# Kernel tuning notes

Measured on AMD Instinct MI355X. Metric: run time of the kernel, lower is better.

The kernel has to match this reference:

```python
import jax, jax.numpy as jnp
import numpy as np

MIN_NORM = 1e-15
PROJ_EPS = 4e-3  # float32 boundary eps used by hgcn PoincareBall.proj
C = 1.0          # curvature for every layer
N, E, D = 10000, 320000, 256


def _norm(x):
    return jnp.maximum(jnp.linalg.norm(x, axis=-1, keepdims=True), MIN_NORM)


def artanh(x):
    return jnp.arctanh(jnp.clip(x, -1 + 1e-7, 1 - 1e-7))


def proj(x, c):
    norm = _norm(x)
    maxnorm = (1.0 - PROJ_EPS) / jnp.sqrt(c)
    return jnp.where(norm > maxnorm, x / norm * maxnorm, x)


def expmap0(u, c):
    sqrt_c = jnp.sqrt(c)
    u_norm = _norm(u)
    return jnp.tanh(sqrt_c * u_norm) * u / (sqrt_c * u_norm)


def logmap0(p, c):
    sqrt_c = jnp.sqrt(c)
    p_norm = _norm(p)
    return artanh(sqrt_c * p_norm) * p / (sqrt_c * p_norm)


def mobius_add(x, y, c):
    x2 = jnp.sum(x * x, -1, keepdims=True)
    y2 = jnp.sum(y * y, -1, keepdims=True)
    xy = jnp.sum(x * y, -1, keepdims=True)
    num = (1 + 2 * c * xy + c * y2) * x + (1 - c * x2) * y
    denom = 1 + 2 * c * xy + c * c * x2 * y2
    return num / jnp.maximum(denom, MIN_NORM)


def mobius_matvec(m, x, c):
    sqrt_c = jnp.sqrt(c)
    x_norm = _norm(x)
    mx = x @ m.T
    mx_norm = _norm(mx)
    res = jnp.tanh(mx_norm / x_norm * artanh(sqrt_c * x_norm)) * mx / (mx_norm * sqrt_c)
    zero_row = jnp.all(mx == 0, axis=-1, keepdims=True)
    return jnp.where(zero_row, jnp.zeros_like(res), res)


def hgc_layer(h, W, b, edge_weight, edge_src, edge_dst, c):
    # HypLinear (dropout=0, eval mode)
    res = proj(mobius_matvec(W, h, c), c)
    hyp_bias = proj(expmap0(b[None, :], c), c)
    h = proj(mobius_add(res, hyp_bias, c), c)
    # HypAgg: tangent-space neighborhood aggregation (spmm over edge list)
    xt = logmap0(h, c)                                  # [N, D]
    msgs = edge_weight[:, None] * xt[edge_src]          # [E, D] irregular gather
    agg = jax.ops.segment_sum(msgs, edge_dst, num_segments=N)
    h = proj(expmap0(agg, c), c)
    # HypAct: relu in tangent space, map back with c_out
    xt = jax.nn.relu(logmap0(h, c))
    return proj(expmap0(xt, c), c)


def setup_inputs() -> dict:
    key = jax.random.key(0)
    ks = jax.random.split(key, 8)
    x = jax.random.normal(ks[0], (N, D), dtype=jnp.float32)
    edge_src = jax.random.randint(ks[1], (E,), 0, N)
    edge_dst = jax.random.randint(ks[2], (E,), 0, N)
    # normalized-adjacency-like positive weights (~1/deg scale)
    edge_weight = jax.random.uniform(ks[3], (E,), dtype=jnp.float32) / 32.0
    s = 1.0 / np.sqrt(D)
    W1 = jax.random.normal(ks[4], (D, D), dtype=jnp.float32) * s
    b1 = jnp.zeros((D,), dtype=jnp.float32)
    W2 = jax.random.normal(ks[5], (D, D), dtype=jnp.float32) * s
    b2 = jnp.zeros((D,), dtype=jnp.float32)
    return {"x": x, "W1": W1, "b1": b1, "W2": W2, "b2": b2,
            "edge_weight": edge_weight, "edge_src": edge_src, "edge_dst": edge_dst}


def reference(x, W1, b1, W2, b2, edge_weight, edge_src, edge_dst):
    # old=True path: map Euclidean features onto the Poincare ball first
    h = proj(expmap0(x, C), C)
    h = hgc_layer(h, W1, b1, edge_weight, edge_src, edge_dst, C)
    h = hgc_layer(h, W2, b2, edge_weight, edge_src, edge_dst, C)
    return h
```

## Files before the change

### kernel.cpp

```cpp
#include <hip/hip_runtime.h>
#include <hip/hip_fp16.h>

#define DIM 256
#define MAXNORM 0.996f
#define MINN 1e-15f
#define CLIPV 0.9999999f
#define CAP 128
#define LDW 264

typedef __attribute__((ext_vector_type(8))) short bf16x8;
typedef __attribute__((ext_vector_type(4))) float f32x4;

__device__ __forceinline__ unsigned short f2bf(float f) {
    unsigned int u = __float_as_uint(f);
    u += 0x7fffu + ((u >> 16) & 1u);
    return (unsigned short)(u >> 16);
}
__device__ __forceinline__ float h2f(unsigned short h) {
    return __half2float(__ushort_as_half(h));
}
__device__ __forceinline__ unsigned short f2h(float f) {
    return __half_as_ushort(__float2half(f));
}
__device__ __forceinline__ float wsum(float v) {
    v += __shfl_xor(v, 32);
    v += __shfl_xor(v, 16);
    v += __shfl_xor(v, 8);
    v += __shfl_xor(v, 4);
    v += __shfl_xor(v, 2);
    v += __shfl_xor(v, 1);
    return v;
}
__device__ __forceinline__ float gsum16(float v) {
    v += __shfl_xor(v, 8);
    v += __shfl_xor(v, 4);
    v += __shfl_xor(v, 2);
    v += __shfl_xor(v, 1);
    return v;
}

__global__ void k_setup(const float* __restrict__ x, unsigned short* __restrict__ h_bf,
                        float* __restrict__ hnorm2, int nrows,
                        int* __restrict__ cnt,
                        const float* __restrict__ W1, const float* __restrict__ W2,
                        unsigned short* __restrict__ w_bf, int nPerW, int eB) {
    int bid = blockIdx.x;
    if (bid < eB) {
        int gid = bid * 256 + threadIdx.x;
        int row = gid >> 6, lane = gid & 63;
        if (row >= nrows) return;
        size_t base = (size_t)row * DIM + lane * 4;
        float4 v = *(const float4*)(x + base);
        float ss = wsum(v.x * v.x + v.y * v.y + v.z * v.z + v.w * v.w);
        float n = fmaxf(sqrtf(ss), MINN);
        float tn = tanhf(n);
        float hn = (tn > MAXNORM) ? MAXNORM : tn;
        float s = hn / n;
        ushort4 ob;
        ob.x = f2bf(v.x * s); ob.y = f2bf(v.y * s);
        ob.z = f2bf(v.z * s); ob.w = f2bf(v.w * s);
        *(ushort4*)(h_bf + base) = ob;
        if (lane == 0) hnorm2[row] = hn * hn;
    } else if (bid < eB + 8) {
        int i = (bid - eB) * 256 + threadIdx.x;
        int stride = 8 * 256;
        for (; i < nrows; i += stride) cnt[i] = 0;
    } else {
        int i = (bid - eB - 8) * 256 + threadIdx.x;
        int stride = 128 * 256;
        for (; i < 2 * nPerW; i += stride)
            w_bf[i] = f2bf(i < nPerW ? W1[i] : W2[i - nPerW]);
    }
}

__global__ void k_fill(const int* __restrict__ esrc, const int* __restrict__ edst,
                       const float* __restrict__ ew, int* __restrict__ cnt,
                       int2* __restrict__ bucket, int nE, int nrows) {
    int e = blockIdx.x * blockDim.x + threadIdx.x;
    if (e >= nE) return;
    int d = edst[e];
    if (d < 0 || d >= nrows) return;
    int pos = atomicAdd(&cnt[d], 1);
    if (pos < CAP)
        bucket[(size_t)d * CAP + pos] = make_int2(esrc[e], __float_as_int(ew[e]));
}

__global__ void k_gemm_post(const unsigned short* __restrict__ Abf,
                            const unsigned short* __restrict__ Wbf,
                            const float* __restrict__ hnorm2,
                            const float* __restrict__ bias,
                            unsigned short* __restrict__ XT, int M) {
    int wave = threadIdx.x >> 6;
    int lane = threadIdx.x & 63;
    int r = lane & 15, oct = lane >> 4;
    int i0 = (blockIdx.x * 4 + wave) * 16;
    int arow = i0 + r;
    bool av = arow < M;
    const unsigned short* ap = Abf + (size_t)(av ? arow : 0) * DIM + oct * 8;
    const unsigned short* wp = Wbf + (size_t)r * DIM + oct * 8;
    const bf16x8 zf = {0, 0, 0, 0, 0, 0, 0, 0};
    f32x4 acc[16];
#pragma unroll
    for (int jt = 0; jt < 16; ++jt) acc[jt] = (f32x4){0.f, 0.f, 0.f, 0.f};
    for (int k0 = 0; k0 < 256; k0 += 32) {
        bf16x8 a = av ? *(const bf16x8*)(ap + k0) : zf;
#pragma unroll
        for (int jt = 0; jt < 16; ++jt) {
            bf16x8 w = *(const bf16x8*)(wp + (size_t)jt * 16 * DIM + k0);
            acc[jt] = __builtin_amdgcn_mfma_f32_16x16x32_bf16(a, w, acc[jt], 0, 0, 0);
        }
    }
    float bv[16];
    float bss = 0.f;
#pragma unroll
    for (int jt = 0; jt < 16; ++jt) {
        bv[jt] = bias[jt * 16 + r];
        bss = fmaf(bv[jt], bv[jt], bss);
    }
    bss = gsum16(bss);
    float bn = fmaxf(sqrtf(bss), MINN);
    float btn = tanhf(bn);
    float bhn = (btn > MAXNORM) ? MAXNORM : btn;
    float bscale = bhn / bn;
    float y2 = bhn * bhn;
#pragma unroll
    for (int jt = 0; jt < 16; ++jt) bv[jt] *= bscale;

#pragma unroll
    for (int q = 0; q < 4; ++q) {
        int row = i0 + oct * 4 + q;
        float sm = 0.f, sxy = 0.f;
#pragma unroll
        for (int jt = 0; jt < 16; ++jt) {
            float m = acc[jt][q];
            sm  = fmaf(m, m, sm);
            sxy = fmaf(m, bv[jt], sxy);
        }
        sm = gsum16(sm);
        sxy = gsum16(sxy);
        if (row < M) {
            float sh = hnorm2[row];
            float xn = fmaxf(sqrtf(sh), MINN);
            float at = atanhf(fminf(xn, CLIPV));
            float mn = fmaxf(sqrtf(sm), MINN);
            float t = tanhf(mn / xn * at);
            float alpha = t / mn;
            float resn = t;
            if (t > MAXNORM) { alpha = MAXNORM / mn; resn = MAXNORM; }
            float x2 = resn * resn;
            float xy = alpha * sxy;
            float Aa = 1.f + 2.f * xy + y2;
            float Bb = 1.f - x2;
            float den = fmaxf(1.f + 2.f * xy + x2 * y2, MINN);
            float s_m = Aa * alpha / den;
            float s_b = Bb / den;
            float hn2 = (Aa * Aa * x2 + 2.f * Aa * Bb * xy + Bb * Bb * y2) / (den * den);
            float hn = fmaxf(sqrtf(fmaxf(hn2, 0.f)), MINN);
            if (hn > MAXNORM) { float f = MAXNORM / hn; s_m *= f; s_b *= f; hn = MAXNORM; }
            float lt = atanhf(fminf(hn, CLIPV)) / hn;
            s_m *= lt; s_b *= lt;
#pragma unroll
            for (int jt = 0; jt < 16; ++jt)
                XT[(size_t)row * DIM + jt * 16 + r] = f2h(fmaf(s_m, acc[jt][q], s_b * bv[jt]));
        }
    }
}

__global__ void __launch_bounds__(256) k_fused(
                        const unsigned short* __restrict__ XT,
                        const int* __restrict__ cnt, const int2* __restrict__ bucket,
                        const unsigned short* __restrict__ Wbf,
                        const float* __restrict__ bias,
                        unsigned short* __restrict__ XT2, int M) {
    __shared__ unsigned short ldsA[16][LDW];
    __shared__ float lds_hn2[16];
    __shared__ float lds_sm[4][16];
    __shared__ float lds_sxy[4][16];
    int wave = threadIdx.x >> 6;
    int lane = threadIdx.x & 63;
    int i0 = blockIdx.x * 16;

    for (int i = 0; i < 4; ++i) {
        int row16 = wave * 4 + i;
        int row = i0 + row16;
        if (row >= M) continue;
        int deg = cnt[row];
        if (deg > CAP) deg = CAP;
        const int2* cpk = bucket + (size_t)row * CAP;
        float a0 = 0.f, a1 = 0.f, a2 = 0.f, a3 = 0.f;
        int p = 0;
        for (; p + 7 < deg; p += 8) {
            ushort4 v[8];
            float w[8];
#pragma unroll
            for (int u = 0; u < 8; ++u) {
                int2 pk = cpk[p + u];
                w[u] = __int_as_float(pk.y);
                v[u] = *(const ushort4*)(XT + (size_t)pk.x * DIM + lane * 4);
            }
#pragma unroll
            for (int u = 0; u < 8; ++u) {
                a0 = fmaf(w[u], h2f(v[u].x), a0);
                a1 = fmaf(w[u], h2f(v[u].y), a1);
                a2 = fmaf(w[u], h2f(v[u].z), a2);
                a3 = fmaf(w[u], h2f(v[u].w), a3);
            }
        }
        for (; p < deg; ++p) {
            int2 pk = cpk[p];
            float w = __int_as_float(pk.y);
            ushort4 v = *(const ushort4*)(XT + (size_t)pk.x * DIM + lane * 4);
            a0 = fmaf(w, h2f(v.x), a0); a1 = fmaf(w, h2f(v.y), a1);
            a2 = fmaf(w, h2f(v.z), a2); a3 = fmaf(w, h2f(v.w), a3);
        }
        float ss = wsum(a0 * a0 + a1 * a1 + a2 * a2 + a3 * a3);
        float n = fmaxf(sqrtf(ss), MINN);
        float tn = tanhf(n);
        float hn = (tn > MAXNORM) ? MAXNORM : tn;
        float s1 = hn / n;
        float lt = atanhf(fminf(hn, CLIPV)) / fmaxf(hn, MINN);
        float s2 = lt * s1;
        float x0 = fmaxf(s2 * a0, 0.f), x1 = fmaxf(s2 * a1, 0.f);
        float x2 = fmaxf(s2 * a2, 0.f), x3 = fmaxf(s2 * a3, 0.f);
        float ss2 = wsum(x0 * x0 + x1 * x1 + x2 * x2 + x3 * x3);
        float n2 = fmaxf(sqrtf(ss2), MINN);
        float tn2 = tanhf(n2);
        float hn2c = (tn2 > MAXNORM) ? MAXNORM : tn2;
        float s3 = hn2c / n2;
        ushort4 ob;
        ob.x = f2bf(s3 * x0); ob.y = f2bf(s3 * x1);
        ob.z = f2bf(s3 * x2); ob.w = f2bf(s3 * x3);
        *(ushort4*)&ldsA[row16][lane * 4] = ob;
        if (lane == 0) lds_hn2[row16] = hn2c * hn2c;
    }
    __syncthreads();

    int r = lane & 15, oct = lane >> 4;
    int jtbase = wave * 4;
    const unsigned short* wp = Wbf + (size_t)(jtbase * 16 + r) * DIM + oct * 8;
    f32x4 acc[4];
#pragma unroll
    for (int j = 0; j < 4; ++j) acc[j] = (f32x4){0.f, 0.f, 0.f, 0.f};
#pragma unroll
    for (int k0 = 0; k0 < 256; k0 += 32) {
        bf16x8 a = *(const bf16x8*)&ldsA[r][oct * 8 + k0];
#pragma unroll
        for (int j = 0; j < 4; ++j) {
            bf16x8 w = *(const bf16x8*)(wp + (size_t)j * 16 * DIM + k0);
            acc[j] = __builtin_amdgcn_mfma_f32_16x16x32_bf16(a, w, acc[j], 0, 0, 0);
        }
    }
    float bss = 0.f;
#pragma unroll
    for (int jt = 0; jt < 16; ++jt) {
        float b = bias[jt * 16 + r];
        bss = fmaf(b, b, bss);
    }
    bss = gsum16(bss);
    float bn = fmaxf(sqrtf(bss), MINN);
    float btn = tanhf(bn);
    float bhn = (btn > MAXNORM) ? MAXNORM : btn;
    float bscale = bhn / bn;
    float y2 = bhn * bhn;
    float bvw[4];
#pragma unroll
    for (int j = 0; j < 4; ++j) bvw[j] = bias[(jtbase + j) * 16 + r] * bscale;
#pragma unroll
    for (int q = 0; q < 4; ++q) {
        float sm = 0.f, sxy = 0.f;
#pragma unroll
        for (int j = 0; j < 4; ++j) {
            float m = acc[j][q];
            sm  = fmaf(m, m, sm);
            sxy = fmaf(m, bvw[j], sxy);
        }
        sm = gsum16(sm);
        sxy = gsum16(sxy);
        if (r == 0) {
            lds_sm[wave][oct * 4 + q] = sm;
            lds_sxy[wave][oct * 4 + q] = sxy;
        }
    }
    __syncthreads();
#pragma unroll
    for (int q = 0; q < 4; ++q) {
        int row16 = oct * 4 + q;
        int row = i0 + row16;
        float sm  = lds_sm[0][row16] + lds_sm[1][row16] + lds_sm[2][row16] + lds_sm[3][row16];
        float sxy = lds_sxy[0][row16] + lds_sxy[1][row16] + lds_sxy[2][row16] + lds_sxy[3][row16];
        if (row < M) {
            float sh = lds_hn2[row16];
            float xn = fmaxf(sqrtf(sh), MINN);
            float at = atanhf(fminf(xn, CLIPV));
            float mn = fmaxf(sqrtf(sm), MINN);
            float t = tanhf(mn / xn * at);
            float alpha = t / mn;
            float resn = t;
            if (t > MAXNORM) { alpha = MAXNORM / mn; resn = MAXNORM; }
            float x2 = resn * resn;
            float xy = alpha * sxy;
            float Aa = 1.f + 2.f * xy + y2;
            float Bb = 1.f - x2;
            float den = fmaxf(1.f + 2.f * xy + x2 * y2, MINN);
            float s_m = Aa * alpha / den;
            float s_b = Bb / den;
            float hn2 = (Aa * Aa * x2 + 2.f * Aa * Bb * xy + Bb * Bb * y2) / (den * den);
            float hn = fmaxf(sqrtf(fmaxf(hn2, 0.f)), MINN);
            if (hn > MAXNORM) { float f = MAXNORM / hn; s_m *= f; s_b *= f; hn = MAXNORM; }
            float lt = atanhf(fminf(hn, CLIPV)) / hn;
            s_m *= lt; s_b *= lt;
#pragma unroll
            for (int j = 0; j < 4; ++j)
                XT2[(size_t)row * DIM + (jtbase + j) * 16 + r] =
                    f2h(fmaf(s_m, acc[j][q], s_b * bvw[j]));
        }
    }
}

__global__ void k_agg_finish(const unsigned short* __restrict__ XT, const int* __restrict__ cnt,
                             const int2* __restrict__ bucket,
                             float* __restrict__ OUT, int nrows) {
    int gid = blockIdx.x * blockDim.x + threadIdx.x;
    int row = gid >> 6, lane = gid & 63;
    if (row >= nrows) return;
    int deg = cnt[row];
    if (deg > CAP) deg = CAP;
    const int2* cpk = bucket + (size_t)row * CAP;
    float a0 = 0.f, a1 = 0.f, a2 = 0.f, a3 = 0.f;
    int p = 0;
    for (; p + 7 < deg; p += 8) {
        ushort4 v[8];
        float w[8];
#pragma unroll
        for (int u = 0; u < 8; ++u) {
            int2 pk = cpk[p + u];
            w[u] = __int_as_float(pk.y);
            v[u] = *(const ushort4*)(XT + (size_t)pk.x * DIM + lane * 4);
        }
#pragma unroll
        for (int u = 0; u < 8; ++u) {
            a0 = fmaf(w[u], h2f(v[u].x), a0);
            a1 = fmaf(w[u], h2f(v[u].y), a1);
            a2 = fmaf(w[u], h2f(v[u].z), a2);
            a3 = fmaf(w[u], h2f(v[u].w), a3);
        }
    }
    for (; p < deg; ++p) {
        int2 pk = cpk[p];
        float w = __int_as_float(pk.y);
        ushort4 v = *(const ushort4*)(XT + (size_t)pk.x * DIM + lane * 4);
        a0 = fmaf(w, h2f(v.x), a0); a1 = fmaf(w, h2f(v.y), a1);
        a2 = fmaf(w, h2f(v.z), a2); a3 = fmaf(w, h2f(v.w), a3);
    }
    float ss = wsum(a0 * a0 + a1 * a1 + a2 * a2 + a3 * a3);
    float n = fmaxf(sqrtf(ss), MINN);
    float tn = tanhf(n);
    float hn = (tn > MAXNORM) ? MAXNORM : tn;
    float s1 = hn / n;
    float lt = atanhf(fminf(hn, CLIPV)) / fmaxf(hn, MINN);
    float s2 = lt * s1;
    float x0 = fmaxf(s2 * a0, 0.f), x1 = fmaxf(s2 * a1, 0.f);
    float x2 = fmaxf(s2 * a2, 0.f), x3 = fmaxf(s2 * a3, 0.f);
    float ss2 = wsum(x0 * x0 + x1 * x1 + x2 * x2 + x3 * x3);
    float n2 = fmaxf(sqrtf(ss2), MINN);
    float tn2 = tanhf(n2);
    float hn2c = (tn2 > MAXNORM) ? MAXNORM : tn2;
    float s3 = hn2c / n2;
    size_t base = (size_t)row * DIM + lane * 4;
    *(float4*)(OUT + base) = make_float4(s3 * x0, s3 * x1, s3 * x2, s3 * x3);
}

static inline size_t align256(size_t x) { return (x + 255) & ~(size_t)255; }

extern "C" void kernel_launch(void* const* d_in, const int* in_sizes, int n_in,
                              void* d_out, int out_size, void* d_ws, size_t ws_size,
                              hipStream_t stream) {
    const float* x  = (const float*)d_in[0];
    const float* W1 = (const float*)d_in[1];
    const float* b1 = (const float*)d_in[2];
    const float* W2 = (const float*)d_in[3];
    const float* b2 = (const float*)d_in[4];
    const float* ew = (const float*)d_in[5];
    const int* esrc = (const int*)d_in[6];
    const int* edst = (const int*)d_in[7];
    const int nE = in_sizes[5];
    const int M  = in_sizes[0] / DIM;

    size_t S = (size_t)M * DIM;
    char* base = (char*)d_ws;
    size_t o = 0;
    int2* bucket   = (int2*)(base + o);          o = align256(o + (size_t)M * CAP * 8);
    int* cnt       = (int*)(base + o);           o = align256(o + (size_t)M * 4);
    float* hnorm2  = (float*)(base + o);         o = align256(o + (size_t)(M + 64) * 4);
    unsigned short* xt   = (unsigned short*)(base + o);  o = align256(o + S * 2);
    unsigned short* xt2  = (unsigned short*)(base + o);  o = align256(o + S * 2);
    unsigned short* h_bf = (unsigned short*)(base + o);  o = align256(o + S * 2);
    unsigned short* w_bf = (unsigned short*)(base + o);  o = align256(o + (size_t)2 * DIM * DIM * 2);

    int rowBlocks = (M + 3) / 4;
    int edgeBlocks = (nE + 255) / 256;

    k_setup<<<rowBlocks + 8 + 128, 256, 0, stream>>>(
        x, h_bf, hnorm2, M, cnt, W1, W2, w_bf, DIM * DIM, rowBlocks);
    k_fill<<<edgeBlocks, 256, 0, stream>>>(esrc, edst, ew, cnt, bucket, nE, M);
    k_gemm_post<<<(M + 63) / 64, 256, 0, stream>>>(h_bf, w_bf, hnorm2, b1, xt, M);
    k_fused<<<(M + 15) / 16, 256, 0, stream>>>(
        xt, cnt, bucket, w_bf + (size_t)DIM * DIM, b2, xt2, M);
    k_agg_finish<<<rowBlocks, 256, 0, stream>>>(xt2, cnt, bucket, (float*)d_out, M);
}
```

Baseline: 200.8 us.

## Restructure fused agg+GEMM kernel to 8 rows per block with 8 waves

The fused aggregation/GEMM kernel now processes 8 rows per block using 512 threads, with one wave per row for the gather instead of each wave looping over 4 rows. The MFMA stage splits the 16 output column tiles across 8 waves (2 each), and the 16-row A tile is zero-padded in its upper half. This is meant to raise parallelism and latency hiding in the irregular gather stage. In exchange, half of the MFMA work is wasted on padding rows, and the W tile is reloaded by twice as many blocks.

```diff
diff --git a/kernel.cpp b/kernel.cpp
--- a/kernel.cpp
+++ b/kernel.cpp
@@ -166,89 +166,94 @@
     }
 }
 
-__global__ void __launch_bounds__(256) k_fused(
+__global__ void __launch_bounds__(512) k_fused(
                         const unsigned short* __restrict__ XT,
                         const int* __restrict__ cnt, const int2* __restrict__ bucket,
                         const unsigned short* __restrict__ Wbf,
                         const float* __restrict__ bias,
                         unsigned short* __restrict__ XT2, int M) {
     __shared__ unsigned short ldsA[16][LDW];
-    __shared__ float lds_hn2[16];
-    __shared__ float lds_sm[4][16];
-    __shared__ float lds_sxy[4][16];
+    __shared__ float lds_hn2[8];
+    __shared__ float lds_sm[8][16];
+    __shared__ float lds_sxy[8][16];
     int wave = threadIdx.x >> 6;
     int lane = threadIdx.x & 63;
-    int i0 = blockIdx.x * 16;
-
-    for (int i = 0; i < 4; ++i) {
-        int row16 = wave * 4 + i;
-        int row = i0 + row16;
-        if (row >= M) continue;
-        int deg = cnt[row];
-        if (deg > CAP) deg = CAP;
-        const int2* cpk = bucket + (size_t)row * CAP;
-        float a0 = 0.f, a1 = 0.f, a2 = 0.f, a3 = 0.f;
-        int p = 0;
-        for (; p + 7 < deg; p += 8) {
-            ushort4 v[8];
-            float w[8];
-#pragma unroll
-            for (int u = 0; u < 8; ++u) {
-                int2 pk = cpk[p + u];
-                w[u] = __int_as_float(pk.y);
-                v[u] = *(const ushort4*)(XT + (size_t)pk.x * DIM + lane * 4);
+    int i0 = blockIdx.x * 8;
+
+    {
+        ushort4 z; z.x = z.y = z.z = z.w = 0;
+        *(ushort4*)&ldsA[wave + 8][lane * 4] = z;
+
+        int row = i0 + wave;
+        if (row < M) {
+            int deg = cnt[row];
+            if (deg > CAP) deg = CAP;
+            const int2* cpk = bucket + (size_t)row * CAP;
+            float a0 = 0.f, a1 = 0.f, a2 = 0.f, a3 = 0.f;
+            int p = 0;
+            for (; p + 7 < deg; p += 8) {
+                ushort4 v[8];
+                float w[8];
+#pragma unroll
+                for (int u = 0; u < 8; ++u) {
+                    int2 pk = cpk[p + u];
+                    w[u] = __int_as_float(pk.y);
+                    v[u] = *(const ushort4*)(XT + (size_t)pk.x * DIM + lane * 4);
+                }
+#pragma unroll
+                for (int u = 0; u < 8; ++u) {
+                    a0 = fmaf(w[u], h2f(v[u].x), a0);
+                    a1 = fmaf(w[u], h2f(v[u].y), a1);
+                    a2 = fmaf(w[u], h2f(v[u].z), a2);
+                    a3 = fmaf(w[u], h2f(v[u].w), a3);
+                }
             }
-#pragma unroll
-            for (int u = 0; u < 8; ++u) {
-                a0 = fmaf(w[u], h2f(v[u].x), a0);
-                a1 = fmaf(w[u], h2f(v[u].y), a1);
-                a2 = fmaf(w[u], h2f(v[u].z), a2);
-                a3 = fmaf(w[u], h2f(v[u].w), a3);
+            for (; p < deg; ++p) {
+                int2 pk = cpk[p];
+                float w = __int_as_float(pk.y);
+                ushort4 v = *(const ushort4*)(XT + (size_t)pk.x * DIM + lane * 4);
+                a0 = fmaf(w, h2f(v.x), a0); a1 = fmaf(w, h2f(v.y), a1);
+                a2 = fmaf(w, h2f(v.z), a2); a3 = fmaf(w, h2f(v.w), a3);
             }
-        }
-        for (; p < deg; ++p) {
-            int2 pk = cpk[p];
-            float w = __int_as_float(pk.y);
-            ushort4 v = *(const ushort4*)(XT + (size_t)pk.x * DIM + lane * 4);
-            a0 = fmaf(w, h2f(v.x), a0); a1 = fmaf(w, h2f(v.y), a1);
-            a2 = fmaf(w, h2f(v.z), a2); a3 = fmaf(w, h2f(v.w), a3);
-        }
-        float ss = wsum(a0 * a0 + a1 * a1 + a2 * a2 + a3 * a3);
-        float n = fmaxf(sqrtf(ss), MINN);
-        float tn = tanhf(n);
-        float hn = (tn > MAXNORM) ? MAXNORM : tn;
-        float s1 = hn / n;
-        float lt = atanhf(fminf(hn, CLIPV)) / fmaxf(hn, MINN);
-        float s2 = lt * s1;
-        float x0 = fmaxf(s2 * a0, 0.f), x1 = fmaxf(s2 * a1, 0.f);
-        float x2 = fmaxf(s2 * a2, 0.f), x3 = fmaxf(s2 * a3, 0.f);
-        float ss2 = wsum(x0 * x0 + x1 * x1 + x2 * x2 + x3 * x3);
-        float n2 = fmaxf(sqrtf(ss2), MINN);
-        float tn2 = tanhf(n2);
-        float hn2c = (tn2 > MAXNORM) ? MAXNORM : tn2;
-        float s3 = hn2c / n2;
-        ushort4 ob;
-        ob.x = f2bf(s3 * x0); ob.y = f2bf(s3 * x1);
-        ob.z = f2bf(s3 * x2); ob.w = f2bf(s3 * x3);
-        *(ushort4*)&ldsA[row16][lane * 4] = ob;
-        if (lane == 0) lds_hn2[row16] = hn2c * hn2c;
+            float ss = wsum(a0 * a0 + a1 * a1 + a2 * a2 + a3 * a3);
+            float n = fmaxf(sqrtf(ss), MINN);
+            float tn = tanhf(n);
+            float hn = (tn > MAXNORM) ? MAXNORM : tn;
+            float s1 = hn / n;
+            float lt = atanhf(fminf(hn, CLIPV)) / fmaxf(hn, MINN);
+            float s2 = lt * s1;
+            float x0 = fmaxf(s2 * a0, 0.f), x1 = fmaxf(s2 * a1, 0.f);
+            float x2 = fmaxf(s2 * a2, 0.f), x3 = fmaxf(s2 * a3, 0.f);
+            float ss2 = wsum(x0 * x0 + x1 * x1 + x2 * x2 + x3 * x3);
+            float n2 = fmaxf(sqrtf(ss2), MINN);
+            float tn2 = tanhf(n2);
+            float hn2c = (tn2 > MAXNORM) ? MAXNORM : tn2;
+            float s3 = hn2c / n2;
+            ushort4 ob;
+            ob.x = f2bf(s3 * x0); ob.y = f2bf(s3 * x1);
+            ob.z = f2bf(s3 * x2); ob.w = f2bf(s3 * x3);
+            *(ushort4*)&ldsA[wave][lane * 4] = ob;
+            if (lane == 0) lds_hn2[wave] = hn2c * hn2c;
+        } else {
+            *(ushort4*)&ldsA[wave][lane * 4] = z;
+            if (lane == 0) lds_hn2[wave] = 0.f;
+        }
     }
     __syncthreads();
 
     int r = lane & 15, oct = lane >> 4;
-    int jtbase = wave * 4;
-    const unsigned short* wp = Wbf + (size_t)(jtbase * 16 + r) * DIM + oct * 8;
-    f32x4 acc[4];
-#pragma unroll
-    for (int j = 0; j < 4; ++j) acc[j] = (f32x4){0.f, 0.f, 0.f, 0.f};
+    int jt0 = wave * 2, jt1 = wave * 2 + 1;
+    const unsigned short* wp0 = Wbf + (size_t)(jt0 * 16 + r) * DIM + oct * 8;
+    const unsigned short* wp1 = Wbf + (size_t)(jt1 * 16 + r) * DIM + oct * 8;
+    f32x4 acc0 = {0.f, 0.f, 0.f, 0.f};
+    f32x4 acc1 = {0.f, 0.f, 0.f, 0.f};
 #pragma unroll
     for (int k0 = 0; k0 < 256; k0 += 32) {
         bf16x8 a = *(const bf16x8*)&ldsA[r][oct * 8 + k0];
-#pragma unroll
-        for (int j = 0; j < 4; ++j) {
-            bf16x8 w = *(const bf16x8*)(wp + (size_t)j * 16 * DIM + k0);
-            acc[j] = __builtin_amdgcn_mfma_f32_16x16x32_bf16(a, w, acc[j], 0, 0, 0);
-        }
+        bf16x8 w0 = *(const bf16x8*)(wp0 + k0);
+        bf16x8 w1 = *(const bf16x8*)(wp1 + k0);
+        acc0 = __builtin_amdgcn_mfma_f32_16x16x32_bf16(a, w0, acc0, 0, 0, 0);
+        acc1 = __builtin_amdgcn_mfma_f32_16x16x32_bf16(a, w1, acc1, 0, 0, 0);
     }
     float bss = 0.f;
 #pragma unroll
@@ -262,20 +267,13 @@
     float bhn = (btn > MAXNORM) ? MAXNORM : btn;
     float bscale = bhn / bn;
     float y2 = bhn * bhn;
-    float bvw[4];
-#pragma unroll
-    for (int j = 0; j < 4; ++j) bvw[j] = bias[(jtbase + j) * 16 + r] * bscale;
+    float bc0 = bias[jt0 * 16 + r] * bscale;
+    float bc1 = bias[jt1 * 16 + r] * bscale;
 #pragma unroll
     for (int q = 0; q < 4; ++q) {
-        float sm = 0.f, sxy = 0.f;
-#pragma unroll
-        for (int j = 0; j < 4; ++j) {
-            float m = acc[j][q];
-            sm  = fmaf(m, m, sm);
-            sxy = fmaf(m, bvw[j], sxy);
-        }
-        sm = gsum16(sm);
-        sxy = gsum16(sxy);
+        float m0 = acc0[q], m1 = acc1[q];
+        float sm  = gsum16(m0 * m0 + m1 * m1);
+        float sxy = gsum16(m0 * bc0 + m1 * bc1);
         if (r == 0) {
             lds_sm[wave][oct * 4 + q] = sm;
             lds_sxy[wave][oct * 4 + q] = sxy;
@@ -286,9 +284,13 @@
     for (int q = 0; q < 4; ++q) {
         int row16 = oct * 4 + q;
         int row = i0 + row16;
-        float sm  = lds_sm[0][row16] + lds_sm[1][row16] + lds_sm[2][row16] + lds_sm[3][row16];
-        float sxy = lds_sxy[0][row16] + lds_sxy[1][row16] + lds_sxy[2][row16] + lds_sxy[3][row16];
-        if (row < M) {
+        if (row16 < 8 && row < M) {
+            float sm = 0.f, sxy = 0.f;
+#pragma unroll
+            for (int w8 = 0; w8 < 8; ++w8) {
+                sm  += lds_sm[w8][row16];
+                sxy += lds_sxy[w8][row16];
+            }
             float sh = lds_hn2[row16];
             float xn = fmaxf(sqrtf(sh), MINN);
             float at = atanhf(fminf(xn, CLIPV));
@@ -309,10 +311,9 @@
             if (hn > MAXNORM) { float f = MAXNORM / hn; s_m *= f; s_b *= f; hn = MAXNORM; }
             float lt = atanhf(fminf(hn, CLIPV)) / hn;
             s_m *= lt; s_b *= lt;
-#pragma unroll
-            for (int j = 0; j < 4; ++j)
-                XT2[(size_t)row * DIM + (jtbase + j) * 16 + r] =
-                    f2h(fmaf(s_m, acc[j][q], s_b * bvw[j]));
+            size_t rb = (size_t)row * DIM;
+            XT2[rb + jt0 * 16 + r] = f2h(fmaf(s_m, acc0[q], s_b * bc0));
+            XT2[rb + jt1 * 16 + r] = f2h(fmaf(s_m, acc1[q], s_b * bc1));
         }
     }
 }
@@ -404,7 +405,7 @@
         x, h_bf, hnorm2, M, cnt, W1, W2, w_bf, DIM * DIM, rowBlocks);
     k_fill<<<edgeBlocks, 256, 0, stream>>>(esrc, edst, ew, cnt, bucket, nE, M);
     k_gemm_post<<<(M + 63) / 64, 256, 0, stream>>>(h_bf, w_bf, hnorm2, b1, xt, M);
-    k_fused<<<(M + 15) / 16, 256, 0, stream>>>(
+    k_fused<<<(M + 7) / 8, 512, 0, stream>>>(
         xt, cnt, bucket, w_bf + (size_t)DIM * DIM, b2, xt2, M);
     k_agg_finish<<<rowBlocks, 256, 0, stream>>>(xt2, cnt, bucket, (float*)d_out, M);
 }
```

New measurement: 215.4 us. +7.3%, slower.
